# Kernel optimization log

Hardware: AMD Instinct MI355X
Metric: run time of the kernel (lower is better)

Reference implementation:

```python
import jax, jax.numpy as jnp
import numpy as np

# graph sizes: G graphs of N_PER nodes each (block-diagonal batched graph)
G, N_PER, F, NHID, E_PER = 128, 512, 128, 128, 4096
N = G * N_PER
E = G * E_PER
L1, L2, L3 = 4, 2, 2            # PANConv filter sizes (conv1 uses init filter_size=4)
K1, K2, K3 = N_PER // 2, N_PER // 4, N_PER // 8  # ratio=0.5 top-k per pooling stage


def setup_inputs() -> dict:
    ks = jax.random.split(jax.random.key(0), 10)
    rng = np.random.default_rng(0)
    off = (np.arange(G) * N_PER)[:, None]
    src = (rng.integers(0, N_PER, size=(G, E_PER)) + off).reshape(-1)
    dst = (rng.integers(0, N_PER, size=(G, E_PER)) + off).reshape(-1)
    edge_index = jnp.asarray(np.stack([src, dst]).astype(np.int32))
    batch = jnp.repeat(jnp.arange(G, dtype=jnp.int32), N_PER)
    def w(k, shp, fan):
        return jax.random.normal(k, shp, jnp.float32) / np.float32(np.sqrt(fan))
    z = lambda *s: jnp.zeros(s, jnp.float32)
    return dict(
        x=jax.random.normal(ks[0], (N, F), jnp.float32),
        edge_index=edge_index, batch=batch,
        lump_W=w(ks[1], (F, NHID), F), lump_b=z(NHID),
        conv1_W=w(ks[2], (NHID, NHID), NHID), conv1_b=z(NHID),
        conv2_W=w(ks[3], (NHID, NHID), NHID), conv2_b=z(NHID),
        conv3_W=w(ks[4], (NHID, NHID), NHID), conv3_b=z(NHID),
        pool1_p=w(ks[5], (NHID,), NHID), pool1_beta=jnp.full((2,), 0.5, jnp.float32),
        pool2_p=w(ks[6], (NHID,), NHID), pool2_beta=jnp.full((2,), 0.5, jnp.float32),
        pool3_p=w(ks[7], (NHID,), NHID), pool3_beta=jnp.full((2,), 0.5, jnp.float32),
        lin1_W=w(ks[8], (NHID, NHID // 2), NHID), lin1_b=z(NHID // 2),
        lin2_W=w(ks[9], (NHID // 2, 1), NHID // 2), lin2_b=z(1),
    )


def _pan_prop(h, src, dst, ew, L):
    # (sum_{l=0..L} A^l) @ h, A weighted by edge weights ew, via iterated gather/scatter
    acc, y = h, h
    n = h.shape[0]
    for _ in range(L):
        y = jax.ops.segment_sum(y[src] * ew[:, None], dst, num_segments=n)
        acc = acc + y
    return acc


def _pan_conv(x, src, dst, ew, W, b, L):
    # PANConv: M = Z^{-1/2} (sum_{l<=L} A^l) Z^{-1/2};  out = M x W + b
    d = _pan_prop(jnp.ones((x.shape[0], 1), x.dtype), src, dst, ew, L)[:, 0]
    dinv = jax.lax.rsqrt(jnp.maximum(d, 1e-12))
    h = dinv[:, None] * _pan_prop(dinv[:, None] * x, src, dst, ew, L)
    return h @ W + b


def _pan_pool(x, src, dst, ew, p, beta, n_per, k):
    # PANPooling: score = beta0*(x.p)/||p|| + beta1*node_strength; per-graph top-k
    n = x.shape[0]
    deg = jax.ops.segment_sum(ew, dst, num_segments=n)
    score = beta[0] * (x @ p) / jnp.linalg.norm(p) + beta[1] * deg
    _, idx = jax.lax.top_k(score.reshape(G, n_per), k)          # [G, k] local indices
    perm = (idx + (jnp.arange(G) * n_per)[:, None]).reshape(-1)  # [G*k] global
    x_new = x[perm] * jnp.tanh(score[perm])[:, None]
    inv = jnp.zeros((n,), jnp.int32).at[perm].set(jnp.arange(G * k, dtype=jnp.int32))
    mask = jnp.zeros((n,), x.dtype).at[perm].set(1.0)
    # keep edge arrays fixed-size: dropped edges get weight 0 (same math as filtering)
    return x_new, inv[src], inv[dst], ew * mask[src] * mask[dst], perm


def reference(x, edge_index, batch, lump_W, lump_b, conv1_W, conv1_b, conv2_W, conv2_b,
              conv3_W, conv3_b, pool1_p, pool1_beta, pool2_p, pool2_beta, pool3_p,
              pool3_beta, lin1_W, lin1_b, lin2_W, lin2_b):
    src, dst = edge_index[0], edge_index[1]
    ew = jnp.ones((src.shape[0],), x.dtype)
    h = x @ lump_W + lump_b                                   # PANLump lift
    h = _pan_conv(h, src, dst, ew, conv1_W, conv1_b, L1)
    h, src, dst, ew, perm1 = _pan_pool(h, src, dst, ew, pool1_p, pool1_beta, N_PER, K1)
    h = _pan_conv(h, src, dst, ew, conv2_W, conv2_b, L2)
    h, src, dst, ew, perm2 = _pan_pool(h, src, dst, ew, pool2_p, pool2_beta, K1, K2)
    h = _pan_conv(h, src, dst, ew, conv3_W, conv3_b, L3)
    h, src, dst, ew, perm3 = _pan_pool(h, src, dst, ew, pool3_p, pool3_beta, K2, K3)
    seg = jnp.repeat(jnp.arange(G, dtype=jnp.int32), K3)
    mean = jax.ops.segment_sum(h, seg, num_segments=G) / jnp.float32(K3)  # scatter_mean
    out = jax.nn.relu(mean @ lin1_W + lin1_b) @ lin2_W + lin2_b           # [G, 1]
    return out
```

## Files before the change

### kernel.cpp

```cpp
#include <hip/hip_runtime.h>
#include <math.h>

#define G_     128
#define E_     524288
#define EPG    4096
#define DEGMAX 48

typedef __attribute__((ext_vector_type(8))) short bf16x8;
typedef __attribute__((ext_vector_type(4))) float f32x4;
typedef __attribute__((ext_vector_type(4))) unsigned short u16x4;

__device__ inline void split_bf16(float x, short& hi, short& lo){
    unsigned u = __float_as_uint(x);
    hi = (short)(u >> 16);
    float hf = __uint_as_float(u & 0xffff0000u);
    unsigned r = __float_as_uint(x - hf);
    lo = (short)(r >> 16);
}

template<int WAVES>
__device__ void gemm_body(char* smem, int bid, const float* __restrict__ X,
        const float* __restrict__ W, const float* __restrict__ bias, float* __restrict__ Y,
        const float* __restrict__ p, const float* __restrict__ beta,
        const int* __restrict__ cntv, float* __restrict__ score){
    short* wsh = (short*)smem;
    short* wsl = (short*)(smem + 34816);
    float* bsh = (float*)(smem + 69632);
    float* qs  = (float*)(smem + 70144);
    float* rednorm = (float*)(smem + 70656);
    const int NT = WAVES*64;
    int t = threadIdx.x;
    for (int e = t; e < 16384; e += NT){
        int k = e >> 7, n = e & 127;
        short hi, lo; split_bf16(W[e], hi, lo);
        wsh[n*136 + k] = hi; wsl[n*136 + k] = lo;
    }
    if (t < 128) bsh[t] = bias[t];
    if (score && t < 64){ float a = p[t], b = p[t+64]; rednorm[t] = a*a + b*b; }
    __syncthreads();
    float b1 = 0.f;
    if (score){
        if (t == 0){ float s = 0.f; for (int i = 0; i < 64; i++) s += rednorm[i]; rednorm[0] = sqrtf(s); }
        __syncthreads();
        if (t < 128) qs[t] = beta[0] * p[t] / rednorm[0];
        b1 = beta[1];
        __syncthreads();
    }
    int wave = t >> 6, lane = t & 63;
    int ln = lane & 15, q = lane >> 4;
    size_t rb = (size_t)bid * (WAVES*16);
    const float* xrow = &X[(rb + wave*16 + ln)*128 + q*8];
    f32x4 acc[8];
    #pragma unroll
    for (int i = 0; i < 8; i++) acc[i] = (f32x4){0.f,0.f,0.f,0.f};
    #pragma unroll
    for (int kc = 0; kc < 4; kc++){
        float4 xa = *(const float4*)(xrow + kc*32);
        float4 xb = *(const float4*)(xrow + kc*32 + 4);
        bf16x8 ah, al; short hi, lo;
        split_bf16(xa.x, hi, lo); ah[0]=hi; al[0]=lo;
        split_bf16(xa.y, hi, lo); ah[1]=hi; al[1]=lo;
        split_bf16(xa.z, hi, lo); ah[2]=hi; al[2]=lo;
        split_bf16(xa.w, hi, lo); ah[3]=hi; al[3]=lo;
        split_bf16(xb.x, hi, lo); ah[4]=hi; al[4]=lo;
        split_bf16(xb.y, hi, lo); ah[5]=hi; al[5]=lo;
        split_bf16(xb.z, hi, lo); ah[6]=hi; al[6]=lo;
        split_bf16(xb.w, hi, lo); ah[7]=hi; al[7]=lo;
        #pragma unroll
        for (int nt = 0; nt < 8; nt++){
            int wo = (nt*16 + ln)*136 + kc*32 + q*8;
            bf16x8 bh = *(const bf16x8*)&wsh[wo];
            bf16x8 bl = *(const bf16x8*)&wsl[wo];
            acc[nt] = __builtin_amdgcn_mfma_f32_16x16x32_bf16(ah, bh, acc[nt], 0, 0, 0);
            acc[nt] = __builtin_amdgcn_mfma_f32_16x16x32_bf16(ah, bl, acc[nt], 0, 0, 0);
            acc[nt] = __builtin_amdgcn_mfma_f32_16x16x32_bf16(al, bh, acc[nt], 0, 0, 0);
        }
    }
    #pragma unroll
    for (int nt = 0; nt < 8; nt++){
        int c = nt*16 + ln;
        float bb = bsh[c];
        #pragma unroll
        for (int r = 0; r < 4; r++){
            Y[(rb + wave*16 + q*4 + r)*128 + c] = acc[nt][r] + bb;
        }
    }
    if (score){
        #pragma unroll
        for (int r = 0; r < 4; r++){
            float sp = 0.f;
            #pragma unroll
            for (int nt = 0; nt < 8; nt++){
                int c = nt*16 + ln;
                sp += (acc[nt][r] + bsh[c]) * qs[c];
            }
            sp += __shfl_xor(sp, 1);
            sp += __shfl_xor(sp, 2);
            sp += __shfl_xor(sp, 4);
            sp += __shfl_xor(sp, 8);
            if (ln == 0){
                int row = (int)rb + wave*16 + q*4 + r;
                score[row] = sp + b1 * (float)cntv[row];
            }
        }
    }
}

__device__ void prep1_body(char* smem, int g, const int* __restrict__ ei,
        int* __restrict__ cnt, unsigned short* __restrict__ csrcp,
        int* __restrict__ permg, float* __restrict__ dinvg){
    int*   lcnt  = (int*)smem;
    float* y     = (float*)(smem + 2048);
    int*   bins  = (int*)(smem + 6144);
    int*   permS = (int*)(smem + 6400);
    int t = threadIdx.x, gbase = g*512;
    lcnt[t] = 0;
    if (t < 64) bins[t] = 0;
    __syncthreads();
    for (int i = t; i < EPG; i += 512){
        int e = g*EPG + i;
        int sv = ei[e] & 511;
        int d  = ei[E_ + e] & 511;
        int slot = atomicAdd(&lcnt[d], 1);
        if (slot < DEGMAX) csrcp[(size_t)(gbase + d)*DEGMAX + slot] = (unsigned short)sv;
    }
    __syncthreads();
    int rawc = lcnt[t];
    cnt[gbase + t] = rawc;
    int dc = min(rawc, DEGMAX);
    {
        int e4 = (dc + 3) & ~3;
        for (int s2 = dc; s2 < e4; s2++) csrcp[(size_t)(gbase + t)*DEGMAX + s2] = 0;
    }
    atomicAdd(&bins[dc], 1);
    __syncthreads();
    if (t < 64){
        int v0 = bins[t], s = v0;
        #pragma unroll
        for (int off = 1; off < 64; off <<= 1){
            int n = __shfl_up(s, off);
            if (t >= off) s += n;
        }
        bins[t] = s - v0;
    }
    __syncthreads();
    {
        int slot = atomicAdd(&bins[dc], 1);
        int pk = t | (dc << 16);
        permS[slot] = pk;
        permg[gbase + slot] = pk;
    }
    __syncthreads();
    int pk = permS[t];
    int pv = pk & 0xffff, pd = pk >> 16;
    y[pv] = 1.f;
    __syncthreads();
    float dacc = 1.f;
    int cur = 0;
    for (int l = 0; l < 4; l++){
        const float* la = &y[cur*512];
        float s = 0.f;
        int nq = (pd + 3) >> 2;
        const u16x4* cp = (const u16x4*)(csrcp + (size_t)(gbase + pv)*DEGMAX);
        u16x4 oc = cp[0];
        #pragma unroll 1
        for (int jq = 0; jq < nq; jq++){
            u16x4 ocn = cp[jq + 1];
            s += (la[(int)oc[0]] + la[(int)oc[1]]) + (la[(int)oc[2]] + la[(int)oc[3]]);
            oc = ocn;
        }
        if (nq) s -= (float)(nq*4 - pd) * la[0];
        y[(1^cur)*512 + pv] = s;
        dacc += s;
        __syncthreads();
        cur ^= 1;
    }
    dinvg[gbase + pv] = rsqrtf(fmaxf(dacc, 1e-12f));
}

__global__ __launch_bounds__(512) void k_lump_prep(const float* __restrict__ x,
        const float* __restrict__ lumpW, const float* __restrict__ lumpb, float* __restrict__ A,
        const int* __restrict__ ei, int* __restrict__ cnt, unsigned short* __restrict__ csr1,
        int* __restrict__ perm1, float* __restrict__ dinv1){
    __shared__ __align__(16) char smem[70912];
    if (blockIdx.x < G_) prep1_body(smem, blockIdx.x, ei, cnt, csr1, perm1, dinv1);
    else gemm_body<8>(smem, blockIdx.x - G_, x, lumpW, lumpb, A,
                      nullptr, nullptr, nullptr, nullptr);
}

template<int WAVES>
__global__ __launch_bounds__(WAVES*64) void k_gemm_mfma(const float* __restrict__ X,
        const float* __restrict__ W, const float* __restrict__ bias, float* __restrict__ Y,
        const float* __restrict__ p, const float* __restrict__ beta,
        const int* __restrict__ cntv, float* __restrict__ score){
    __shared__ __align__(16) char smem[70912];
    gemm_body<WAVES>(smem, blockIdx.x, X, W, bias, Y, p, beta, cntv, score);
}

template<int NPER, int L, int IT, bool SEL>
__global__ __launch_bounds__(1024)
void k_prop(const int* __restrict__ permg, const float* __restrict__ dinvg,
        const unsigned short* __restrict__ csrcp,
        const float* __restrict__ X, const int* __restrict__ selg,
        const float* __restrict__ thg, float* __restrict__ OUT){
    __shared__ __align__(16) float y[NPER*32];
    __shared__ float dinvs[NPER];
    int g = blockIdx.x, fq = blockIdx.y, gbase = g*NPER;
    int t = threadIdx.x;
    int f4 = (t & 7)*4;
    int fo = fq*32 + f4;
    if (t < NPER) dinvs[t] = dinvg[gbase + t];
    int pkr[IT];
    {
        int wv = t >> 6, gi = (t >> 3) & 7;
        #pragma unroll
        for (int it = 0; it < IT; it++){
            int ch = (it & 1) ? (15 - wv) : wv;
            pkr[it] = permg[gbase + (16*it + ch)*8 + gi];
        }
    }
    __syncthreads();
    float4 acc[IT];
    #pragma unroll
    for (int it = 0; it < IT; it++){
        int v = pkr[it] & 0xffff;
        float d = dinvs[v];
        size_t row;
        if (SEL){
            row = (size_t)selg[gbase + v];
            d *= thg[gbase + v];
        } else {
            row = (size_t)(gbase + v);
        }
        float4 w = *(const float4*)&X[row*128 + fo];
        w.x*=d; w.y*=d; w.z*=d; w.w*=d;
        acc[it] = w;
        *(float4*)&y[v*32 + f4] = w;
    }
    __syncthreads();
    for (int l = 0; l < L; l++){
        float4 s[IT];
        #pragma unroll
        for (int it = 0; it < IT; it++){
            int pk = pkr[it];
            int c = pk >> 16;
            int nq = (c + 3) >> 2;
            const u16x4* cp = (const u16x4*)(csrcp + (size_t)(gbase + (pk & 0xffff))*DEGMAX);
            float4 ss = make_float4(0.f,0.f,0.f,0.f);
            u16x4 oc = cp[0];
            #pragma unroll 1
            for (int jq = 0; jq < nq; jq++){
                u16x4 ocn = cp[jq + 1];
                float4 w0 = *(const float4*)&y[((int)oc[0])*32 + f4];
                float4 w1 = *(const float4*)&y[((int)oc[1])*32 + f4];
                float4 w2 = *(const float4*)&y[((int)oc[2])*32 + f4];
                float4 w3 = *(const float4*)&y[((int)oc[3])*32 + f4];
                ss.x += (w0.x + w1.x) + (w2.x + w3.x);
                ss.y += (w0.y + w1.y) + (w2.y + w3.y);
                ss.z += (w0.z + w1.z) + (w2.z + w3.z);
                ss.w += (w0.w + w1.w) + (w2.w + w3.w);
                oc = ocn;
            }
            if (nq){
                float fp = (float)(nq*4 - c);
                float4 z = *(const float4*)&y[f4];
                ss.x -= fp*z.x; ss.y -= fp*z.y; ss.z -= fp*z.z; ss.w -= fp*z.w;
            }
            s[it] = ss;
        }
        __syncthreads();
        #pragma unroll
        for (int it = 0; it < IT; it++){
            int v = pkr[it] & 0xffff;
            *(float4*)&y[v*32 + f4] = s[it];
            acc[it].x+=s[it].x; acc[it].y+=s[it].y; acc[it].z+=s[it].z; acc[it].w+=s[it].w;
        }
        __syncthreads();
    }
    #pragma unroll
    for (int it = 0; it < IT; it++){
        int v = pkr[it] & 0xffff;
        float d = dinvs[v];
        float4 w = acc[it];
        w.x*=d; w.y*=d; w.z*=d; w.w*=d;
        *(float4*)&OUT[(size_t)(gbase + v)*128 + fo] = w;
    }
}

template<int NPER, bool BUILD>
__global__ __launch_bounds__(512) void k_pooltop(const float* __restrict__ score_in,
        const int* __restrict__ esrc_in, const int* __restrict__ edst_in,
        int* __restrict__ esrc_out, int* __restrict__ edst_out,
        int* __restrict__ cnt_next, unsigned short* __restrict__ csrcp,
        int* __restrict__ permg, float* __restrict__ dinvg,
        int* __restrict__ selg, float* __restrict__ thg){
    __shared__ __align__(16) float sc[NPER];
    __shared__ int  nid[NPER];
    __shared__ int  lcnt[NPER/2];
    __shared__ int  bins[64];
    __shared__ int  permS[NPER/2];
    const int K = NPER/2;
    int g = blockIdx.x, t = threadIdx.x, gbase = g*NPER;
    if (t < K) lcnt[t] = 0;
    if (t < 64) bins[t] = 0;
    if (t < NPER) sc[t] = score_in[gbase + t];
    __syncthreads();
    if (t < NPER){
        float s = sc[t];
        int rank = 0;
        const float4* sc4 = (const float4*)sc;
        #pragma unroll 8
        for (int j4 = 0; j4 < NPER/4; j4++){
            float4 v = sc4[j4];
            int j = j4*4;
            rank += (v.x > s) || (v.x == s && (j+0) < t);
            rank += (v.y > s) || (v.y == s && (j+1) < t);
            rank += (v.z > s) || (v.z == s && (j+2) < t);
            rank += (v.w > s) || (v.w == s && (j+3) < t);
        }
        if (rank < K){
            nid[t] = g*K + rank;
            selg[g*K + rank] = gbase + t;
            thg[g*K + rank]  = tanhf(s);
        } else nid[t] = -1;
    }
    __syncthreads();
    if (BUILD){
        for (int i = t; i < EPG; i += 512){
            int e = g*EPG + i;
            int d = edst_in[e];
            if (d < 0) continue;
            int s_ = esrc_in[e];
            int ns = nid[s_ - gbase], nd = nid[d - gbase];
            if ((ns | nd) < 0){ edst_out[e] = -1; }
            else {
                esrc_out[e] = ns; edst_out[e] = nd;
                int slot = atomicAdd(&lcnt[nd & (K-1)], 1);
                if (slot < DEGMAX) csrcp[(size_t)nd*DEGMAX + slot] = (unsigned short)(ns & (K-1));
            }
        }
        __syncthreads();
        float* yd = sc;
        int rawc = 0, dc = 0;
        if (t < K){
            rawc = lcnt[t];
            cnt_next[g*K + t] = rawc;
            dc = min(rawc, DEGMAX);
            int e4 = (dc + 3) & ~3;
            for (int s2 = dc; s2 < e4; s2++) csrcp[(size_t)(g*K + t)*DEGMAX + s2] = 0;
            atomicAdd(&bins[dc], 1);
        }
        __syncthreads();
        if (t < 64){
            int v0 = bins[t], s = v0;
            #pragma unroll
            for (int off = 1; off < 64; off <<= 1){
                int n = __shfl_up(s, off);
                if (t >= off) s += n;
            }
            bins[t] = s - v0;
        }
        __syncthreads();
        if (t < K){
            int slot = atomicAdd(&bins[dc], 1);
            permS[slot] = t | (dc << 16);
            permg[g*K + slot] = permS[slot];
        }
        __syncthreads();
        int pv = 0, pd = 0;
        if (t < K){
            int pk = permS[t];
            pv = pk & 0xffff; pd = pk >> 16;
            yd[pv] = 1.f;
        }
        __syncthreads();
        float dacc = 1.f;
        int cur = 0;
        for (int l = 0; l < 2; l++){
            if (t < K){
                const float* la = &yd[cur*K];
                float s = 0.f;
                int nq = (pd + 3) >> 2;
                const u16x4* cp = (const u16x4*)(csrcp + (size_t)(g*K + pv)*DEGMAX);
                u16x4 oc = cp[0];
                #pragma unroll 1
                for (int jq = 0; jq < nq; jq++){
                    u16x4 ocn = cp[jq + 1];
                    s += (la[(int)oc[0]] + la[(int)oc[1]]) + (la[(int)oc[2]] + la[(int)oc[3]]);
                    oc = ocn;
                }
                if (nq) s -= (float)(nq*4 - pd) * la[0];
                yd[(1^cur)*K + pv] = s;
                dacc += s;
            }
            __syncthreads();
            cur ^= 1;
        }
        if (t < K) dinvg[g*K + pv] = rsqrtf(fmaxf(dacc, 1e-12f));
    }
}

__global__ __launch_bounds__(128) void k_pool3_mean(const float* __restrict__ score_in,
        const float* __restrict__ h, const float* __restrict__ W1, const float* __restrict__ b1,
        const float* __restrict__ W2, const float* __restrict__ b2, float* __restrict__ out){
    __shared__ __align__(16) float sc[128];
    __shared__ int   selS[64];
    __shared__ float thS[64];
    __shared__ float mr[128];
    int g = blockIdx.x, t = threadIdx.x;
    sc[t] = score_in[g*128 + t];
    __syncthreads();
    {
        float s = sc[t];
        int rank = 0;
        const float4* sc4 = (const float4*)sc;
        #pragma unroll 8
        for (int j4 = 0; j4 < 32; j4++){
            float4 v = sc4[j4];
            int j = j4*4;
            rank += (v.x > s) || (v.x == s && (j+0) < t);
            rank += (v.y > s) || (v.y == s && (j+1) < t);
            rank += (v.z > s) || (v.z == s && (j+2) < t);
            rank += (v.w > s) || (v.w == s && (j+3) < t);
        }
        if (rank < 64){ selS[rank] = g*128 + t; thS[rank] = tanhf(s); }
    }
    __syncthreads();
    float s = 0.f;
    #pragma unroll 8
    for (int r = 0; r < 64; r++) s += h[(size_t)selS[r]*128 + t] * thS[r];
    mr[t] = s * (1.f/64.f);
    __syncthreads();
    if (t < 64){
        float a = b1[t];
        #pragma unroll 8
        for (int k = 0; k < 128; k++) a += mr[k]*W1[k*64 + t];
        a = fmaxf(a, 0.f);
        float r = a * W2[t];
        #pragma unroll
        for (int off = 32; off > 0; off >>= 1) r += __shfl_down(r, off);
        if (t == 0) out[g] = r + b2[0];
    }
}

extern "C" void kernel_launch(void* const* d_in, const int* in_sizes, int n_in,
                              void* d_out, int out_size, void* d_ws, size_t ws_size,
                              hipStream_t stream){
    (void)in_sizes; (void)n_in; (void)out_size; (void)ws_size;
    const float* x     = (const float*)d_in[0];
    const int*   ei    = (const int*)d_in[1];
    const float* lumpW = (const float*)d_in[3];
    const float* lumpb = (const float*)d_in[4];
    const float* convW[3]    = {(const float*)d_in[5], (const float*)d_in[7], (const float*)d_in[9]};
    const float* convB[3]    = {(const float*)d_in[6], (const float*)d_in[8], (const float*)d_in[10]};
    const float* poolP[3]    = {(const float*)d_in[11], (const float*)d_in[13], (const float*)d_in[15]};
    const float* poolBeta[3] = {(const float*)d_in[12], (const float*)d_in[14], (const float*)d_in[16]};
    const float* lin1W = (const float*)d_in[17];
    const float* lin1b = (const float*)d_in[18];
    const float* lin2W = (const float*)d_in[19];
    const float* lin2b = (const float*)d_in[20];
    float* out = (float*)d_out;

    char* w8 = (char*)d_ws;
    size_t off = 0;
    auto alloc = [&](size_t bytes)->char*{
        char* p = w8 + off; off += (bytes + 255) & ~(size_t)255; return p;
    };
    float* A     = (float*)alloc((size_t)65536*128*4);
    float* Bb    = (float*)alloc((size_t)65536*128*4);
    int*   srcA  = (int*)alloc((size_t)E_*4);
    int*   dstA  = (int*)alloc((size_t)E_*4);
    unsigned short* csr1 = (unsigned short*)alloc((size_t)65536*DEGMAX*2);
    unsigned short* csr2 = (unsigned short*)alloc((size_t)32768*DEGMAX*2);
    unsigned short* csr3 = (unsigned short*)alloc((size_t)16384*DEGMAX*2);
    int*   cntA  = (int*)alloc((size_t)(65536+32768+16384)*4);
    int*   cnt1 = cntA, *cnt2 = cntA + 65536, *cnt3 = cntA + 98304;
    int*   perm1 = (int*)alloc((size_t)65536*4);
    int*   perm2 = (int*)alloc((size_t)32768*4);
    int*   perm3 = (int*)alloc((size_t)16384*4);
    float* dinv1 = (float*)alloc((size_t)65536*4);
    float* dinv2 = (float*)alloc((size_t)32768*4);
    float* dinv3 = (float*)alloc((size_t)16384*4);
    float* score1 = (float*)alloc((size_t)65536*4);
    float* score2 = (float*)alloc((size_t)32768*4);
    float* score3 = (float*)alloc((size_t)16384*4);
    int*   sel2  = (int*)alloc((size_t)32768*4);
    int*   sel3  = (int*)alloc((size_t)16384*4);
    float* th2   = (float*)alloc((size_t)32768*4);
    float* th3   = (float*)alloc((size_t)16384*4);

    k_lump_prep<<<G_ + 512, 512, 0, stream>>>(x, lumpW, lumpb, A, ei, cnt1, csr1, perm1, dinv1);

    k_prop<512,4,4,false><<<dim3(G_,4), 1024, 0, stream>>>(perm1, dinv1, csr1, A,
            nullptr, nullptr, Bb);
    k_gemm_mfma<8><<<512, 512, 0, stream>>>(Bb, convW[0], convB[0], A,
            poolP[0], poolBeta[0], cnt1, score1);
    k_pooltop<512,true><<<G_, 512, 0, stream>>>(score1, ei, ei + E_, srcA, dstA,
            cnt2, csr2, perm2, dinv2, sel2, th2);

    k_prop<256,2,2,true><<<dim3(G_,4), 1024, 0, stream>>>(perm2, dinv2, csr2, A,
            sel2, th2, Bb);
    k_gemm_mfma<8><<<256, 512, 0, stream>>>(Bb, convW[1], convB[1], A,
            poolP[1], poolBeta[1], cnt2, score2);
    k_pooltop<256,true><<<G_, 512, 0, stream>>>(score2, srcA, dstA, srcA, dstA,
            cnt3, csr3, perm3, dinv3, sel3, th3);

    k_prop<128,2,1,true><<<dim3(G_,4), 1024, 0, stream>>>(perm3, dinv3, csr3, A,
            sel3, th3, Bb);
    k_gemm_mfma<4><<<256, 256, 0, stream>>>(Bb, convW[2], convB[2], A,
            poolP[2], poolBeta[2], cnt3, score3);

    k_pool3_mean<<<G_, 128, 0, stream>>>(score3, A, lin1W, lin1b, lin2W, lin2b, out);
}
```

Measured before the change: 300.0 us.

## Stage CSR neighbor lists in LDS and fuse final GEMM with pool/readout

In k_prop, each block now copies its graph's compacted CSR neighbor lists into shared memory, using a wave prefix scan to compute offsets. The L propagation iterations then read indices from LDS instead of re-reading global memory. The last conv GEMM, pool-3 top-k, mean and MLP head are merged into one per-graph kernel (k_stage3) that keeps the GEMM output in LDS. This removes one launch and the global round trip of h and score3, but it raises LDS use per block and adds setup syncs and serial copy loops to k_prop.

```diff
diff --git a/kernel.cpp b/kernel.cpp
--- a/kernel.cpp
+++ b/kernel.cpp
@@ -203,8 +203,13 @@
         const unsigned short* __restrict__ csrcp,
         const float* __restrict__ X, const int* __restrict__ selg,
         const float* __restrict__ thg, float* __restrict__ OUT){
+    constexpr int QMAX = (EPG + 3*NPER)/4 + 4;
+    constexpr int NW   = NPER/64;
     __shared__ __align__(16) float y[NPER*32];
     __shared__ float dinvs[NPER];
+    __shared__ u16x4 csrl[QMAX];
+    __shared__ unsigned short qoffS[NPER];
+    __shared__ int wsumS[NW];
     int g = blockIdx.x, fq = blockIdx.y, gbase = g*NPER;
     int t = threadIdx.x;
     int f4 = (t & 7)*4;
@@ -219,7 +224,32 @@
             pkr[it] = permg[gbase + (16*it + ch)*8 + gi];
         }
     }
-    __syncthreads();
+    int nqv = 0, pvv = 0;
+    if (t < NPER){
+        int pk2 = permg[gbase + t];
+        pvv = pk2 & 0xffff;
+        nqv = ((pk2 >> 16) + 3) >> 2;
+    }
+    int incl = nqv;
+    #pragma unroll
+    for (int off2 = 1; off2 < 64; off2 <<= 1){
+        int n2 = __shfl_up(incl, off2);
+        if ((t & 63) >= off2) incl += n2;
+    }
+    if (t < NPER && (t & 63) == 63) wsumS[t >> 6] = incl;
+    __syncthreads();
+    if (t == 0){
+        int run = 0;
+        #pragma unroll
+        for (int w = 0; w < NW; w++){ int v2 = wsumS[w]; wsumS[w] = run; run += v2; }
+    }
+    __syncthreads();
+    if (t < NPER){
+        int qo = incl - nqv + wsumS[t >> 6];
+        qoffS[pvv] = (unsigned short)qo;
+        const u16x4* gp = (const u16x4*)(csrcp + (size_t)(gbase + pvv)*DEGMAX);
+        for (int j = 0; j < nqv; j++) csrl[qo + j] = gp[j];
+    }
     float4 acc[IT];
     #pragma unroll
     for (int it = 0; it < IT; it++){
@@ -243,9 +273,10 @@
         #pragma unroll
         for (int it = 0; it < IT; it++){
             int pk = pkr[it];
+            int v = pk & 0xffff;
             int c = pk >> 16;
             int nq = (c + 3) >> 2;
-            const u16x4* cp = (const u16x4*)(csrcp + (size_t)(gbase + (pk & 0xffff))*DEGMAX);
+            const u16x4* cp = &csrl[(int)qoffS[v]];
             float4 ss = make_float4(0.f,0.f,0.f,0.f);
             u16x4 oc = cp[0];
             #pragma unroll 1
@@ -400,20 +431,99 @@
     }
 }
 
-__global__ __launch_bounds__(128) void k_pool3_mean(const float* __restrict__ score_in,
-        const float* __restrict__ h, const float* __restrict__ W1, const float* __restrict__ b1,
-        const float* __restrict__ W2, const float* __restrict__ b2, float* __restrict__ out){
-    __shared__ __align__(16) float sc[128];
+__global__ __launch_bounds__(512) void k_stage3(const float* __restrict__ X,
+        const float* __restrict__ W, const float* __restrict__ bias,
+        const float* __restrict__ p, const float* __restrict__ beta,
+        const int* __restrict__ cntv,
+        const float* __restrict__ W1, const float* __restrict__ b1,
+        const float* __restrict__ W2, const float* __restrict__ b2,
+        float* __restrict__ out){
+    __shared__ __align__(16) char smem[70912];
+    __shared__ float scs[128];
+    __shared__ float thS[64];
     __shared__ int   selS[64];
-    __shared__ float thS[64];
     __shared__ float mr[128];
+    short* wsh = (short*)smem;
+    short* wsl = (short*)(smem + 34816);
+    float* bsh = (float*)(smem + 69632);
+    float* qs  = (float*)(smem + 70144);
+    float* rednorm = (float*)(smem + 70656);
     int g = blockIdx.x, t = threadIdx.x;
-    sc[t] = score_in[g*128 + t];
-    __syncthreads();
-    {
-        float s = sc[t];
+    for (int e = t; e < 16384; e += 512){
+        int k = e >> 7, n = e & 127;
+        short hi, lo; split_bf16(W[e], hi, lo);
+        wsh[n*136 + k] = hi; wsl[n*136 + k] = lo;
+    }
+    if (t < 128) bsh[t] = bias[t];
+    if (t < 64){ float a = p[t], b = p[t+64]; rednorm[t] = a*a + b*b; }
+    __syncthreads();
+    if (t == 0){ float s = 0.f; for (int i = 0; i < 64; i++) s += rednorm[i]; rednorm[0] = sqrtf(s); }
+    __syncthreads();
+    if (t < 128) qs[t] = beta[0] * p[t] / rednorm[0];
+    float b1v = beta[1];
+    __syncthreads();
+    int wave = t >> 6, lane = t & 63;
+    int ln = lane & 15, q = lane >> 4;
+    const float* xrow = &X[((size_t)g*128 + wave*16 + ln)*128 + q*8];
+    f32x4 acc[8];
+    #pragma unroll
+    for (int i = 0; i < 8; i++) acc[i] = (f32x4){0.f,0.f,0.f,0.f};
+    #pragma unroll
+    for (int kc = 0; kc < 4; kc++){
+        float4 xa = *(const float4*)(xrow + kc*32);
+        float4 xb = *(const float4*)(xrow + kc*32 + 4);
+        bf16x8 ah, al; short hi, lo;
+        split_bf16(xa.x, hi, lo); ah[0]=hi; al[0]=lo;
+        split_bf16(xa.y, hi, lo); ah[1]=hi; al[1]=lo;
+        split_bf16(xa.z, hi, lo); ah[2]=hi; al[2]=lo;
+        split_bf16(xa.w, hi, lo); ah[3]=hi; al[3]=lo;
+        split_bf16(xb.x, hi, lo); ah[4]=hi; al[4]=lo;
+        split_bf16(xb.y, hi, lo); ah[5]=hi; al[5]=lo;
+        split_bf16(xb.z, hi, lo); ah[6]=hi; al[6]=lo;
+        split_bf16(xb.w, hi, lo); ah[7]=hi; al[7]=lo;
+        #pragma unroll
+        for (int nt = 0; nt < 8; nt++){
+            int wo = (nt*16 + ln)*136 + kc*32 + q*8;
+            bf16x8 bh = *(const bf16x8*)&wsh[wo];
+            bf16x8 bl = *(const bf16x8*)&wsl[wo];
+            acc[nt] = __builtin_amdgcn_mfma_f32_16x16x32_bf16(ah, bh, acc[nt], 0, 0, 0);
+            acc[nt] = __builtin_amdgcn_mfma_f32_16x16x32_bf16(ah, bl, acc[nt], 0, 0, 0);
+            acc[nt] = __builtin_amdgcn_mfma_f32_16x16x32_bf16(al, bh, acc[nt], 0, 0, 0);
+        }
+    }
+    #pragma unroll
+    for (int r = 0; r < 4; r++){
+        float sp = 0.f;
+        #pragma unroll
+        for (int nt = 0; nt < 8; nt++){
+            int c = nt*16 + ln;
+            sp += (acc[nt][r] + bsh[c]) * qs[c];
+        }
+        sp += __shfl_xor(sp, 1);
+        sp += __shfl_xor(sp, 2);
+        sp += __shfl_xor(sp, 4);
+        sp += __shfl_xor(sp, 8);
+        if (ln == 0){
+            int rl = wave*16 + q*4 + r;
+            scs[rl] = sp + b1v * (float)cntv[g*128 + rl];
+        }
+    }
+    __syncthreads();
+    float* Yl = (float*)smem;
+    #pragma unroll
+    for (int nt = 0; nt < 8; nt++){
+        int c = nt*16 + ln;
+        float bb = bsh[c];
+        #pragma unroll
+        for (int r = 0; r < 4; r++){
+            Yl[(wave*16 + q*4 + r)*132 + c] = acc[nt][r] + bb;
+        }
+    }
+    __syncthreads();
+    if (t < 128){
+        float s = scs[t];
         int rank = 0;
-        const float4* sc4 = (const float4*)sc;
+        const float4* sc4 = (const float4*)scs;
         #pragma unroll 8
         for (int j4 = 0; j4 < 32; j4++){
             float4 v = sc4[j4];
@@ -423,13 +533,15 @@
             rank += (v.z > s) || (v.z == s && (j+2) < t);
             rank += (v.w > s) || (v.w == s && (j+3) < t);
         }
-        if (rank < 64){ selS[rank] = g*128 + t; thS[rank] = tanhf(s); }
-    }
-    __syncthreads();
-    float s = 0.f;
-    #pragma unroll 8
-    for (int r = 0; r < 64; r++) s += h[(size_t)selS[r]*128 + t] * thS[r];
-    mr[t] = s * (1.f/64.f);
+        if (rank < 64){ selS[rank] = t; thS[rank] = tanhf(s); }
+    }
+    __syncthreads();
+    if (t < 128){
+        float s = 0.f;
+        #pragma unroll 8
+        for (int r = 0; r < 64; r++) s += Yl[selS[r]*132 + t] * thS[r];
+        mr[t] = s * (1.f/64.f);
+    }
     __syncthreads();
     if (t < 64){
         float a = b1[t];
@@ -483,7 +595,6 @@
     float* dinv3 = (float*)alloc((size_t)16384*4);
     float* score1 = (float*)alloc((size_t)65536*4);
     float* score2 = (float*)alloc((size_t)32768*4);
-    float* score3 = (float*)alloc((size_t)16384*4);
     int*   sel2  = (int*)alloc((size_t)32768*4);
     int*   sel3  = (int*)alloc((size_t)16384*4);
     float* th2   = (float*)alloc((size_t)32768*4);
@@ -507,8 +618,6 @@
 
     k_prop<128,2,1,true><<<dim3(G_,4), 1024, 0, stream>>>(perm3, dinv3, csr3, A,
             sel3, th3, Bb);
-    k_gemm_mfma<4><<<256, 256, 0, stream>>>(Bb, convW[2], convB[2], A,
-            poolP[2], poolBeta[2], cnt3, score3);
-
-    k_pool3_mean<<<G_, 128, 0, stream>>>(score3, A, lin1W, lin1b, lin2W, lin2b, out);
-}
+    k_stage3<<<G_, 512, 0, stream>>>(Bb, convW[2], convB[2],
+            poolP[2], poolBeta[2], cnt3, lin1W, lin1b, lin2W, lin2b, out);
+}
```

Result: no change. 298.0 us (-0.7%).
